# Kernel optimization log

Measured on AMD Instinct MI355X. Metric: run time of the kernel, lower is better.

## Reference

```python
import jax, jax.numpy as jnp
import numpy as np

B = 32; L = 512; D_MODEL = 512; N_LAYERS = 4
D_STATE = 64; D_CONV = 4; EXPAND = 2; HEADDIM = 64; PRED = 96
D_INNER = EXPAND * D_MODEL            # 1024
NHEADS = D_INNER // HEADDIM           # 16
CONV_DIM = D_INNER + 2 * D_STATE      # 1152
D_IN_PROJ = 2 * D_INNER + 2 * D_STATE + NHEADS  # 2192
EPS = 1e-5


def setup_inputs() -> dict:
    key = jax.random.key(0)
    ks = jax.random.split(key, 8)
    s = lambda k, shape, scale=0.02: jax.random.normal(k, shape, jnp.float32) * scale
    return {
        "x": jax.random.normal(ks[0], (B, L, D_MODEL), jnp.float32),
        "in_proj_w": s(ks[1], (N_LAYERS, D_IN_PROJ, D_MODEL)),
        "conv_w": s(ks[2], (N_LAYERS, CONV_DIM, D_CONV), 0.2),
        "conv_b": jnp.zeros((N_LAYERS, CONV_DIM), jnp.float32),
        "dt_bias": jnp.log(jnp.expm1(jax.random.uniform(ks[3], (N_LAYERS, NHEADS), minval=0.001, maxval=0.1))),
        "A_log": jnp.log(jax.random.uniform(ks[4], (N_LAYERS, NHEADS), minval=1.0, maxval=16.0)),
        "Dp": jnp.ones((N_LAYERS, NHEADS), jnp.float32),
        "norm_w": jnp.ones((N_LAYERS, D_INNER), jnp.float32),
        "out_proj_w": s(ks[5], (N_LAYERS, D_MODEL, D_INNER)),
        "ln_w": jnp.ones((N_LAYERS, D_MODEL), jnp.float32),
        "ln_b": jnp.zeros((N_LAYERS, D_MODEL), jnp.float32),
        "final_w": s(ks[6], (D_MODEL, D_MODEL)),
        "final_b": jnp.zeros((D_MODEL,), jnp.float32),
    }


def _silu(x):
    return x * jax.nn.sigmoid(x)


def _causal_dwconv(x, w, b):
    # x: (B, L, C); depthwise causal conv, kernel D_CONV, left pad D_CONV-1
    xt = jnp.swapaxes(x, 1, 2)  # (B, C, L)
    y = jax.lax.conv_general_dilated(
        xt, w[:, None, :], window_strides=(1,), padding=[(D_CONV - 1, 0)],
        feature_group_count=CONV_DIM, dimension_numbers=("NCH", "OIH", "NCH"))
    return jnp.swapaxes(y + b[None, :, None], 1, 2)


def _ssd_scan(xh, dt, Bm, Cm, A, Dp):
    # xh: (B,L,H,P), dt: (B,L,H), Bm/Cm: (B,L,N), A/Dp: (H,)
    dA = jnp.exp(dt * A)  # (B,L,H)

    def step(h, t):
        dA_t, x_t, dt_t, B_t, C_t = t  # (B,H), (B,H,P), (B,H), (B,N), (B,N)
        h = h * dA_t[:, :, None, None] + (dt_t[:, :, None] * x_t)[..., None] * B_t[:, None, None, :]
        y = jnp.einsum("bhpn,bn->bhp", h, C_t)
        return h, y

    Bb, Ll, H, P = xh.shape
    N = Bm.shape[-1]
    h0 = jnp.zeros((Bb, H, P, N), xh.dtype)
    xs = (jnp.moveaxis(dA, 1, 0), jnp.moveaxis(xh, 1, 0), jnp.moveaxis(dt, 1, 0),
          jnp.moveaxis(Bm, 1, 0), jnp.moveaxis(Cm, 1, 0))
    _, ys = jax.lax.scan(step, h0, xs)
    y = jnp.moveaxis(ys, 0, 1)  # (B,L,H,P)
    return y + xh * Dp[None, None, :, None]


def _mamba2(x, w_in, cw, cb, dtb, a_log, dp, nw, w_out):
    zxbcdt = jnp.einsum("bld,ed->ble", x, w_in)  # (B,L,D_IN_PROJ)
    z = zxbcdt[..., :D_INNER]
    xBC = zxbcdt[..., D_INNER:D_INNER + CONV_DIM]
    dt = jax.nn.softplus(zxbcdt[..., -NHEADS:] + dtb)
    xBC = _silu(_causal_dwconv(xBC, cw, cb))
    xh = xBC[..., :D_INNER].reshape(x.shape[0], x.shape[1], NHEADS, HEADDIM)
    Bm = xBC[..., D_INNER:D_INNER + D_STATE]
    Cm = xBC[..., D_INNER + D_STATE:]
    A = -jnp.exp(a_log)
    y = _ssd_scan(xh, dt, Bm, Cm, A, dp).reshape(x.shape[0], x.shape[1], D_INNER)
    # gated RMSNorm (norm_before_gate=False): gate first, then normalize
    y = y * _silu(z)
    y = y * jax.lax.rsqrt(jnp.mean(y * y, axis=-1, keepdims=True) + EPS) * nw
    return jnp.einsum("ble,de->bld", y, w_out)


def _layernorm(x, w, b):
    xc = x - jnp.mean(x, axis=-1, keepdims=True)
    return xc * jax.lax.rsqrt(jnp.mean(xc * xc, axis=-1, keepdims=True) + EPS) * w + b


def reference(x, in_proj_w, conv_w, conv_b, dt_bias, A_log, Dp, norm_w,
              out_proj_w, ln_w, ln_b, final_w, final_b):
    h = x
    for i in range(N_LAYERS):
        res = h
        h = _mamba2(h, in_proj_w[i], conv_w[i], conv_b[i], dt_bias[i],
                    A_log[i], Dp[i], norm_w[i], out_proj_w[i])
        h = _layernorm(h + res, ln_w[i], ln_b[i])
        # dropout is identity in eval mode
    h = h[:, -PRED:, :]
    return jnp.einsum("bld,ed->ble", h, final_w) + final_b
```

## Files before the change

kernel.cpp:

```cpp
#include <hip/hip_runtime.h>
#include <stdint.h>

#define BATCH 32
#define SEQ   512
#define DM    512
#define NL    4
#define DSTATE 64
#define DI    1024
#define NH    16
#define HD    64
#define PREDN 96
#define CDIM  1152
#define CSEG  144
#define DPROJ 2192
#define XBW   1168
#define NC    8
#define EPSF  1e-5f

typedef float  f32x4  __attribute__((ext_vector_type(4)));
typedef __bf16 bf16x4 __attribute__((ext_vector_type(4)));
typedef __bf16 bf16x8 __attribute__((ext_vector_type(8)));

__device__ __forceinline__ float sigmoidf_(float x){ return 1.f/(1.f+__expf(-x)); }
__device__ __forceinline__ float siluf_(float x){ return x*sigmoidf_(x); }
__device__ __forceinline__ float softplusf_(float x){ return (x>20.f)?x:log1pf(__expf(x)); }

__device__ __forceinline__ void gld16(const void* g, void* l){
  __builtin_amdgcn_global_load_lds((__attribute__((address_space(1))) void*)g,
                                   (__attribute__((address_space(3))) void*)l, 16, 0, 0);
}

template<typename TC>
__global__ __launch_bounds__(256) void gemm128(
    const __bf16* __restrict__ A, const __bf16* __restrict__ W,
    TC* __restrict__ C, TC* __restrict__ C2, const float* __restrict__ bias,
    int M, int Nreal, int ldc, int ldc2, int splitN, int K, int remapA)
{
  __shared__ __bf16 sAB[2*128*64];
  __bf16* sA = sAB;
  __bf16* sW = sAB + 128*64;
  const int tid  = threadIdx.x;
  const int m0   = blockIdx.x*128, n0 = blockIdx.y*128;
  const int lane = tid&63, wave = tid>>6;
  const int l15  = lane&15, quad = lane>>4;
  const int wr   = (wave>>1)*64, wc = (wave&1)*64;
  f32x4 acc[4][4];
  #pragma unroll
  for (int a=0;a<4;++a)
    #pragma unroll
    for (int b=0;b<4;++b) acc[a][b] = (f32x4){0,0,0,0};

  for (int k0=0; k0<K; k0+=64){
    #pragma unroll
    for (int j=0;j<4;++j){
      const int f = j*256 + tid;
      const int r = f>>3;
      const int kc = (((f&7) ^ (r&7)))*8;
      int ga = m0 + r;
      if (remapA){ int bb = ga/PREDN; ga = bb*SEQ + (SEQ-PREDN) + (ga - bb*PREDN); }
      gld16(A + (size_t)ga*K + k0 + kc, &sA[f*8]);
      int rb = n0 + r; rb = rb < Nreal ? rb : (Nreal-1);
      gld16(W + (size_t)rb*K + k0 + kc, &sW[f*8]);
    }
    __syncthreads();
    #pragma unroll
    for (int kk=0; kk<64; kk+=32){
      const int kcb = (kk>>3) + quad;
      bf16x8 av[4], bv[4];
      #pragma unroll
      for (int mi=0;mi<4;++mi){
        const int row = wr+mi*16+l15;
        av[mi] = *(const bf16x8*)&sA[row*64 + ((kcb ^ (row&7))<<3)];
      }
      #pragma unroll
      for (int ni=0;ni<4;++ni){
        const int row = wc+ni*16+l15;
        bv[ni] = *(const bf16x8*)&sW[row*64 + ((kcb ^ (row&7))<<3)];
      }
      #pragma unroll
      for (int mi=0;mi<4;++mi)
        #pragma unroll
        for (int ni=0;ni<4;++ni)
          acc[mi][ni] = __builtin_amdgcn_mfma_f32_16x16x32_bf16(av[mi],bv[ni],acc[mi][ni],0,0,0);
    }
    __syncthreads();
  }

  if constexpr (sizeof(TC)==2){
    #pragma unroll
    for (int mi=0;mi<4;++mi)
      #pragma unroll
      for (int ni=0;ni<4;++ni)
        #pragma unroll
        for (int r4=0;r4<4;++r4){
          const int row = wr+mi*16+quad*4+r4;
          const int col = wc+ni*16+l15;
          const int g2  = (col>>3) ^ (row&15);
          sAB[row*128 + g2*8 + (col&7)] = (__bf16)acc[mi][ni][r4];
        }
    __syncthreads();
    #pragma unroll
    for (int it=0; it<8; ++it){
      const int idx = it*256 + tid;
      const int row = idx>>4, g = idx&15;
      const int g2 = g ^ (row&15);
      bf16x8 v = *(const bf16x8*)&sAB[row*128 + g2*8];
      const int col0 = n0 + g*8;
      if (col0 < Nreal){
        const int grow = m0 + row;
        if (col0 < splitN) *(bf16x8*)&C [(size_t)grow*ldc  + col0]          = v;
        else               *(bf16x8*)&C2[(size_t)grow*ldc2 + (col0-splitN)] = v;
      }
    }
  } else {
    #pragma unroll
    for (int ni=0;ni<4;++ni){
      const int col = n0 + wc + ni*16 + l15;
      if (col < Nreal){
        const float badd = bias ? bias[col] : 0.f;
        #pragma unroll
        for (int mi=0;mi<4;++mi){
          #pragma unroll
          for (int r4=0;r4<4;++r4){
            const int row = m0 + wr + mi*16 + quad*4 + r4;
            C[(size_t)row*ldc + col] = (TC)(acc[mi][ni][r4] + badd);
          }
        }
      }
    }
  }
}

__global__ __launch_bounds__(256) void cast4_k(
    const float* __restrict__ s0, __bf16* __restrict__ d0, int n0,
    const float* __restrict__ s1, __bf16* __restrict__ d1, int n1,
    const float* __restrict__ s2, __bf16* __restrict__ d2, int n2,
    const float* __restrict__ s3, __bf16* __restrict__ d3, int n3)
{
  int i = blockIdx.x*256 + threadIdx.x;
  const float* s; __bf16* d;
  if (i < n0){ s=s0; d=d0; }
  else if ((i-=n0) < n1){ s=s1; d=d1; }
  else if ((i-=n1) < n2){ s=s2; d=d2; }
  else if ((i-=n2) < n3){ s=s3; d=d3; }
  else return;
  float4 v = ((const float4*)s)[i];
  bf16x4 o;
  o[0]=(__bf16)v.x; o[1]=(__bf16)v.y; o[2]=(__bf16)v.z; o[3]=(__bf16)v.w;
  ((bf16x4*)d)[i] = o;
}

__global__ __launch_bounds__(256) void conv_silu_k(
    const __bf16* __restrict__ xbw, const float* __restrict__ cw,
    const float* __restrict__ cb, __bf16* __restrict__ xout,
    __bf16* __restrict__ bcout)
{
  int idx = blockIdx.x*256 + threadIdx.x;
  if (idx >= BATCH*SEQ*CSEG) return;
  const int seg = idx % CSEG;
  const int bt  = idx / CSEG;
  const int t = bt % SEQ, b = bt / SEQ;
  const int d0 = seg*8;
  const __bf16* src = xbw + ((size_t)b*SEQ + t)*XBW + d0;
  bf16x8 z8;
  #pragma unroll
  for (int e=0;e<8;++e) z8[e]=(__bf16)0.f;
  bf16x8 x3 = *(const bf16x8*)src;
  bf16x8 x2 = (t>=1)? *(const bf16x8*)(src -   XBW) : z8;
  bf16x8 x1 = (t>=2)? *(const bf16x8*)(src - 2*XBW) : z8;
  bf16x8 x0 = (t>=3)? *(const bf16x8*)(src - 3*XBW) : z8;
  const float4* w4  = (const float4*)(cw + (size_t)d0*4);
  const float4* cb4 = (const float4*)(cb + d0);
  float4 cbl = cb4[0], cbh = cb4[1];
  bf16x8 o;
  #pragma unroll
  for (int e=0;e<8;++e){
    float4 w = w4[e];
    float acc = (e<4 ? (&cbl.x)[e] : (&cbh.x)[e-4])
              + w.x*(float)x0[e] + w.y*(float)x1[e]
              + w.z*(float)x2[e] + w.w*(float)x3[e];
    o[e] = (__bf16)siluf_(acc);
  }
  if (d0 < DI) *(bf16x8*)(xout  + ((size_t)b*SEQ+t)*DI  + d0)       = o;
  else         *(bf16x8*)(bcout + ((size_t)b*SEQ+t)*128 + (d0-DI))  = o;
}

__global__ __launch_bounds__(256) void ssd_fused_k(
    const __bf16* __restrict__ bc,
    __bf16* __restrict__ xy,
    const __bf16* __restrict__ xbw,
    const float* __restrict__ dtb_, const float* __restrict__ alog_,
    const float* __restrict__ dp_)
{
  __shared__ __bf16 sPool[5*64*72];
  __bf16* sB   = sPool;
  __bf16* sS   = sPool;
  __bf16* sC   = sPool + 1*64*72;
  __bf16* sXT  = sPool + 2*64*72;
  __bf16* sBwT = sPool + 3*64*72;
  __bf16* sHT  = sPool + 4*64*72;
  __shared__ float sCS[SEQ], sDT[SEQ];
  const int bid = blockIdx.x;
  const int h = bid & 15, b = bid >> 4;
  const int tid = threadIdx.x, wave = tid>>6, lane = tid&63;
  const int l15 = lane&15, quad = lane>>4;
  const int wm = (wave>>1)*32, wn = (wave&1)*32;

  const float Ah  = -__expf(alog_[h]);
  const float dtb = dtb_[h];
  const float Dh  = dp_[h];

  for (int t = tid; t < SEQ; t += 256){
    float raw = (float)xbw[((size_t)b*SEQ + t)*XBW + CDIM + h];
    float dt = softplusf_(raw + dtb);
    sDT[t] = dt;
    sCS[t] = dt*Ah;
  }
  __syncthreads();
  for (int ch = wave; ch < NC; ch += 4){
    float s = sCS[ch*64 + lane];
    #pragma unroll
    for (int off=1; off<64; off<<=1){
      float v = __shfl_up(s, off);
      if (lane >= off) s += v;
    }
    sCS[ch*64 + lane] = s;
  }
  __syncthreads();

  f32x4 run[2][2];
  #pragma unroll
  for (int a=0;a<2;++a)
    #pragma unroll
    for (int d=0;d<2;++d) run[a][d] = (f32x4){0,0,0,0};

  for (int c = 0; c < NC; ++c){
    const int t0 = c*64;
    {
      const int r = tid>>2, seg = (tid&3)*16;
      const __bf16* row = bc + ((size_t)b*SEQ + t0 + r)*128;
      bf16x8 vb0 = *(const bf16x8*)(row + seg);
      bf16x8 vb1 = *(const bf16x8*)(row + seg + 8);
      bf16x8 vc0 = *(const bf16x8*)(row + 64 + seg);
      bf16x8 vc1 = *(const bf16x8*)(row + 64 + seg + 8);
      *(bf16x8*)&sB[r*72+seg]   = vb0;
      *(bf16x8*)&sB[r*72+seg+8] = vb1;
      *(bf16x8*)&sC[r*72+seg]   = vc0;
      *(bf16x8*)&sC[r*72+seg+8] = vc1;
      const float w = __expf(sCS[t0+63] - sCS[t0+r]) * sDT[t0+r];
      #pragma unroll
      for (int e=0;e<8;++e){
        sBwT[(seg+e)*72 + r]   = (__bf16)(w*(float)vb0[e]);
        sBwT[(seg+8+e)*72 + r] = (__bf16)(w*(float)vb1[e]);
      }
      const __bf16* xrow = xy + ((size_t)b*SEQ + t0 + r)*DI + h*64;
      bf16x8 vx0 = *(const bf16x8*)(xrow + seg);
      bf16x8 vx1 = *(const bf16x8*)(xrow + seg + 8);
      #pragma unroll
      for (int e=0;e<8;++e){
        sXT[(seg+e)*72 + r]   = vx0[e];
        sXT[(seg+8+e)*72 + r] = vx1[e];
      }
    }
    __syncthreads();

    f32x4 aS[2][2];
    #pragma unroll
    for (int a=0;a<2;++a)
      #pragma unroll
      for (int d=0;d<2;++d) aS[a][d] = (f32x4){0,0,0,0};
    #pragma unroll
    for (int kk=0; kk<64; kk+=32){
      const int kf = kk + quad*8;
      bf16x8 a0 = *(const bf16x8*)&sC[(wm+l15)*72+kf];
      bf16x8 a1 = *(const bf16x8*)&sC[(wm+16+l15)*72+kf];
      bf16x8 b0 = *(const bf16x8*)&sB[(wn+l15)*72+kf];
      bf16x8 b1 = *(const bf16x8*)&sB[(wn+16+l15)*72+kf];
      aS[0][0] = __builtin_amdgcn_mfma_f32_16x16x32_bf16(a0,b0,aS[0][0],0,0,0);
      aS[0][1] = __builtin_amdgcn_mfma_f32_16x16x32_bf16(a0,b1,aS[0][1],0,0,0);
      aS[1][0] = __builtin_amdgcn_mfma_f32_16x16x32_bf16(a1,b0,aS[1][0],0,0,0);
      aS[1][1] = __builtin_amdgcn_mfma_f32_16x16x32_bf16(a1,b1,aS[1][1],0,0,0);
    }
    __syncthreads();

    #pragma unroll
    for (int mi=0;mi<2;++mi)
      #pragma unroll
      for (int ni=0;ni<2;++ni)
        #pragma unroll
        for (int r4=0;r4<4;++r4){
          const int i = wm+mi*16+quad*4+r4, j = wn+ni*16+l15;
          float ed = __expf(fminf(sCS[t0+i]-sCS[t0+j], 0.f)) * sDT[t0+j];
          float v = aS[mi][ni][r4]*ed;
          sS[i*72+j] = (__bf16)((j<=i)? v : 0.f);
          sHT[j*72+i] = (__bf16)run[mi][ni][r4];
        }
    __syncthreads();

    f32x4 aY[2][2], aH[2][2], aYi[2][2];
    #pragma unroll
    for (int a=0;a<2;++a)
      #pragma unroll
      for (int d=0;d<2;++d){
        aY[a][d]=(f32x4){0,0,0,0}; aH[a][d]=(f32x4){0,0,0,0};
        aYi[a][d]=(f32x4){0,0,0,0};
      }
    #pragma unroll
    for (int kk=0; kk<64; kk+=32){
      const int kf = kk + quad*8;
      bf16x8 b0 = *(const bf16x8*)&sXT[(wn+l15)*72+kf];
      bf16x8 b1 = *(const bf16x8*)&sXT[(wn+16+l15)*72+kf];
      bf16x8 s0 = *(const bf16x8*)&sS[(wm+l15)*72+kf];
      bf16x8 s1 = *(const bf16x8*)&sS[(wm+16+l15)*72+kf];
      bf16x8 w0 = *(const bf16x8*)&sBwT[(wm+l15)*72+kf];
      bf16x8 w1 = *(const bf16x8*)&sBwT[(wm+16+l15)*72+kf];
      bf16x8 c0 = *(const bf16x8*)&sC[(wm+l15)*72+kf];
      bf16x8 c1 = *(const bf16x8*)&sC[(wm+16+l15)*72+kf];
      bf16x8 h0 = *(const bf16x8*)&sHT[(wn+l15)*72+kf];
      bf16x8 h1 = *(const bf16x8*)&sHT[(wn+16+l15)*72+kf];
      aY[0][0] = __builtin_amdgcn_mfma_f32_16x16x32_bf16(s0,b0,aY[0][0],0,0,0);
      aY[0][1] = __builtin_amdgcn_mfma_f32_16x16x32_bf16(s0,b1,aY[0][1],0,0,0);
      aY[1][0] = __builtin_amdgcn_mfma_f32_16x16x32_bf16(s1,b0,aY[1][0],0,0,0);
      aY[1][1] = __builtin_amdgcn_mfma_f32_16x16x32_bf16(s1,b1,aY[1][1],0,0,0);
      aH[0][0] = __builtin_amdgcn_mfma_f32_16x16x32_bf16(w0,b0,aH[0][0],0,0,0);
      aH[0][1] = __builtin_amdgcn_mfma_f32_16x16x32_bf16(w0,b1,aH[0][1],0,0,0);
      aH[1][0] = __builtin_amdgcn_mfma_f32_16x16x32_bf16(w1,b0,aH[1][0],0,0,0);
      aH[1][1] = __builtin_amdgcn_mfma_f32_16x16x32_bf16(w1,b1,aH[1][1],0,0,0);
      aYi[0][0] = __builtin_amdgcn_mfma_f32_16x16x32_bf16(c0,h0,aYi[0][0],0,0,0);
      aYi[0][1] = __builtin_amdgcn_mfma_f32_16x16x32_bf16(c0,h1,aYi[0][1],0,0,0);
      aYi[1][0] = __builtin_amdgcn_mfma_f32_16x16x32_bf16(c1,h0,aYi[1][0],0,0,0);
      aYi[1][1] = __builtin_amdgcn_mfma_f32_16x16x32_bf16(c1,h1,aYi[1][1],0,0,0);
    }

    const float lam = __expf(sCS[t0+63]);
    #pragma unroll
    for (int mi=0;mi<2;++mi)
      #pragma unroll
      for (int ni=0;ni<2;++ni)
        #pragma unroll
        for (int r4=0;r4<4;++r4){
          const int i = wm+mi*16+quad*4+r4;
          const int p = wn+ni*16+l15;
          const float xval = (float)sXT[p*72 + i];
          const float e2 = __expf(sCS[t0+i]);
          const float yv = aY[mi][ni][r4] + Dh*xval + e2*aYi[mi][ni][r4];
          xy[((size_t)b*SEQ + t0 + i)*DI + h*64 + p] = (__bf16)yv;
          run[mi][ni][r4] = run[mi][ni][r4]*lam + aH[mi][ni][r4];
        }
    __syncthreads();
  }
}

__global__ __launch_bounds__(256) void gate_rms_k(
    __bf16* __restrict__ y, const __bf16* __restrict__ z, const float* __restrict__ nw)
{
  __shared__ float red[4];
  const int tid = threadIdx.x;
  const int sub = tid>>7;
  const int off = (tid&127)*8;
  const size_t row = (size_t)blockIdx.x*2 + sub;
  __bf16* yrow = y + row*DI;
  const __bf16* zrow = z + row*DI;
  bf16x8 yv = *(const bf16x8*)(yrow+off);
  bf16x8 zv = *(const bf16x8*)(zrow+off);
  float u[8]; float ss = 0.f;
  #pragma unroll
  for (int e=0;e<8;++e){
    float uu = (float)yv[e]*siluf_((float)zv[e]);
    u[e]=uu; ss += uu*uu;
  }
  #pragma unroll
  for (int o=32;o;o>>=1) ss += __shfl_xor(ss,o);
  if ((tid&63)==0) red[tid>>6] = ss;
  __syncthreads();
  ss = red[sub*2] + red[sub*2+1];
  const float sc = rsqrtf(ss*(1.f/DI) + EPSF);
  const float4* nw4 = (const float4*)(nw + off);
  float4 n0 = nw4[0], n1 = nw4[1];
  bf16x8 o;
  #pragma unroll
  for (int e=0;e<8;++e)
    o[e] = (__bf16)(u[e]*sc*(e<4 ? (&n0.x)[e] : (&n1.x)[e-4]));
  *(bf16x8*)(yrow+off) = o;
}

__global__ __launch_bounds__(256) void add_ln_k(
    const __bf16* __restrict__ tmp, __bf16* __restrict__ resio,
    const float* __restrict__ w, const float* __restrict__ bb)
{
  const int tid = threadIdx.x, lane = tid&63;
  const size_t row = (size_t)blockIdx.x*4 + (tid>>6);
  const int off = lane*8;
  const __bf16* trow = tmp + row*DM;
  __bf16* rrow = resio + row*DM;
  bf16x8 tv = *(const bf16x8*)(trow+off);
  bf16x8 rv = *(const bf16x8*)(rrow+off);
  float v[8]; float s = 0.f;
  #pragma unroll
  for (int e=0;e<8;++e){ v[e]=(float)tv[e]+(float)rv[e]; s += v[e]; }
  #pragma unroll
  for (int o=32;o;o>>=1) s += __shfl_xor(s,o);
  const float mean = s*(1.f/DM);
  float q = 0.f;
  #pragma unroll
  for (int e=0;e<8;++e){ v[e]-=mean; q += v[e]*v[e]; }
  #pragma unroll
  for (int o=32;o;o>>=1) q += __shfl_xor(q,o);
  const float rstd = rsqrtf(q*(1.f/DM) + EPSF);
  const float4* w4 = (const float4*)(w + off);
  const float4* b4 = (const float4*)(bb + off);
  float4 w0=w4[0], w1=w4[1], b0=b4[0], b1=b4[1];
  bf16x8 o8;
  #pragma unroll
  for (int e=0;e<8;++e){
    float we = e<4 ? (&w0.x)[e] : (&w1.x)[e-4];
    float be = e<4 ? (&b0.x)[e] : (&b1.x)[e-4];
    o8[e] = (__bf16)(v[e]*rstd*we + be);
  }
  *(bf16x8*)(rrow+off) = o8;
}

extern "C" void kernel_launch(void* const* d_in, const int* in_sizes, int n_in,
                              void* d_out, int out_size, void* d_ws, size_t ws_size,
                              hipStream_t stream)
{
  const float* x         = (const float*)d_in[0];
  const float* in_proj_w = (const float*)d_in[1];
  const float* conv_w    = (const float*)d_in[2];
  const float* conv_b    = (const float*)d_in[3];
  const float* dt_bias   = (const float*)d_in[4];
  const float* A_log     = (const float*)d_in[5];
  const float* Dp        = (const float*)d_in[6];
  const float* norm_w    = (const float*)d_in[7];
  const float* out_proj_w= (const float*)d_in[8];
  const float* ln_w      = (const float*)d_in[9];
  const float* ln_b      = (const float*)d_in[10];
  const float* final_w   = (const float*)d_in[11];
  const float* final_b   = (const float*)d_in[12];
  float* out = (float*)d_out;

  const size_t ROWS = (size_t)BATCH*SEQ;
  __bf16* wbf_in  = (__bf16*)d_ws;
  __bf16* wbf_out = wbf_in  + (size_t)NL*DPROJ*DM;
  __bf16* wbf_fin = wbf_out + (size_t)NL*DM*DI;
  __bf16* zbuf    = wbf_fin + (size_t)DM*DM;
  __bf16* xbw     = zbuf    + ROWS*DI;
  __bf16* ybuf    = xbw     + ROWS*XBW;
  __bf16* bcb     = ybuf    + ROWS*DI;
  __bf16* xcur    = bcb     + ROWS*128;
  __bf16* tmp  = xbw;

  {
    int n1 = NL*DPROJ*DM/4, n2 = NL*DM*DI/4, n3 = DM*DM/4, n4 = (int)(ROWS*DM/4);
    int tot = n1+n2+n3+n4;
    cast4_k<<<(tot+255)/256, 256, 0, stream>>>(
        in_proj_w, wbf_in, n1, out_proj_w, wbf_out, n2,
        final_w, wbf_fin, n3, x, xcur, n4);
  }

  const int convTotal = BATCH*SEQ*CSEG;
  const int BIGN = 1<<30;

  for (int l=0; l<NL; ++l){
    const __bf16* wl = wbf_in + (size_t)l*DPROJ*DM;
    gemm128<__bf16><<<dim3((int)(ROWS/128), (DPROJ+127)/128), 256, 0, stream>>>(
        xcur, wl, zbuf, xbw, nullptr, (int)ROWS, DPROJ, DI, XBW, DI, DM, 0);
    conv_silu_k<<<(convTotal+255)/256, 256, 0, stream>>>(
        xbw, conv_w + (size_t)l*CDIM*4, conv_b + (size_t)l*CDIM, ybuf, bcb);
    ssd_fused_k<<<BATCH*NH, 256, 0, stream>>>(
        bcb, ybuf, xbw, dt_bias + l*NH, A_log + l*NH, Dp + l*NH);
    gate_rms_k<<<(int)(ROWS/2), 256, 0, stream>>>(ybuf, zbuf, norm_w + (size_t)l*DI);
    gemm128<__bf16><<<dim3((int)(ROWS/128), DM/128), 256, 0, stream>>>(
        ybuf, wbf_out + (size_t)l*DM*DI, tmp, tmp, nullptr, (int)ROWS, DM, DM, DM, BIGN, DI, 0);
    add_ln_k<<<(int)(ROWS/4), 256, 0, stream>>>(tmp, xcur, ln_w + l*DM, ln_b + l*DM);
  }
  gemm128<float><<<dim3((BATCH*PREDN)/128, DM/128), 256, 0, stream>>>(
      xcur, wbf_fin, out, out, final_b, BATCH*PREDN, DM, DM, DM, BIGN, DM, 1);
}
```

Baseline: 835.5 us.

## Fuse gated RMSNorm into SSD epilogue and out-projection GEMM

```diff
diff --git a/kernel.cpp b/kernel.cpp
--- a/kernel.cpp
+++ b/kernel.cpp
@@ -34,6 +34,7 @@
 __global__ __launch_bounds__(256) void gemm128(
     const __bf16* __restrict__ A, const __bf16* __restrict__ W,
     TC* __restrict__ C, TC* __restrict__ C2, const float* __restrict__ bias,
+    const float* __restrict__ rowscale,
     int M, int Nreal, int ldc, int ldc2, int splitN, int K, int remapA)
 {
   __shared__ __bf16 sAB[2*128*64];
@@ -108,6 +109,11 @@
       const int col0 = n0 + g*8;
       if (col0 < Nreal){
         const int grow = m0 + row;
+        if (rowscale){
+          const float s = rsqrtf(rowscale[grow]*(1.f/DI) + EPSF);
+          #pragma unroll
+          for (int e=0;e<8;++e) v[e] = (__bf16)((float)v[e]*s);
+        }
         if (col0 < splitN) *(bf16x8*)&C [(size_t)grow*ldc  + col0]          = v;
         else               *(bf16x8*)&C2[(size_t)grow*ldc2 + (col0-splitN)] = v;
       }
@@ -131,23 +137,46 @@
   }
 }
 
-__global__ __launch_bounds__(256) void cast4_k(
+__global__ __launch_bounds__(256) void cast5_k(
     const float* __restrict__ s0, __bf16* __restrict__ d0, int n0,
     const float* __restrict__ s1, __bf16* __restrict__ d1, int n1,
+    const float* __restrict__ nw_,
     const float* __restrict__ s2, __bf16* __restrict__ d2, int n2,
-    const float* __restrict__ s3, __bf16* __restrict__ d3, int n3)
+    const float* __restrict__ s3, __bf16* __restrict__ d3, int n3,
+    float* __restrict__ z4, int n4)
 {
   int i = blockIdx.x*256 + threadIdx.x;
-  const float* s; __bf16* d;
-  if (i < n0){ s=s0; d=d0; }
-  else if ((i-=n0) < n1){ s=s1; d=d1; }
-  else if ((i-=n1) < n2){ s=s2; d=d2; }
-  else if ((i-=n2) < n3){ s=s3; d=d3; }
-  else return;
-  float4 v = ((const float4*)s)[i];
-  bf16x4 o;
-  o[0]=(__bf16)v.x; o[1]=(__bf16)v.y; o[2]=(__bf16)v.z; o[3]=(__bf16)v.w;
-  ((bf16x4*)d)[i] = o;
+  if (i < n0){
+    float4 v = ((const float4*)s0)[i];
+    bf16x4 o; o[0]=(__bf16)v.x; o[1]=(__bf16)v.y; o[2]=(__bf16)v.z; o[3]=(__bf16)v.w;
+    ((bf16x4*)d0)[i] = o; return;
+  }
+  i -= n0;
+  if (i < n1){
+    float4 v = ((const float4*)s1)[i];
+    const int flat = i*4;
+    const int l = flat / (DM*DI);
+    const int k = flat % DI;
+    float4 w = *(const float4*)(nw_ + l*DI + k);
+    bf16x4 o;
+    o[0]=(__bf16)(v.x*w.x); o[1]=(__bf16)(v.y*w.y);
+    o[2]=(__bf16)(v.z*w.z); o[3]=(__bf16)(v.w*w.w);
+    ((bf16x4*)d1)[i] = o; return;
+  }
+  i -= n1;
+  if (i < n2){
+    float4 v = ((const float4*)s2)[i];
+    bf16x4 o; o[0]=(__bf16)v.x; o[1]=(__bf16)v.y; o[2]=(__bf16)v.z; o[3]=(__bf16)v.w;
+    ((bf16x4*)d2)[i] = o; return;
+  }
+  i -= n2;
+  if (i < n3){
+    float4 v = ((const float4*)s3)[i];
+    bf16x4 o; o[0]=(__bf16)v.x; o[1]=(__bf16)v.y; o[2]=(__bf16)v.z; o[3]=(__bf16)v.w;
+    ((bf16x4*)d3)[i] = o; return;
+  }
+  i -= n3;
+  if (i < n4) ((float4*)z4)[i] = (float4){0,0,0,0};
 }
 
 __global__ __launch_bounds__(256) void conv_silu_k(
@@ -189,8 +218,9 @@
     const __bf16* __restrict__ bc,
     __bf16* __restrict__ xy,
     const __bf16* __restrict__ xbw,
+    const __bf16* __restrict__ zg,
     const float* __restrict__ dtb_, const float* __restrict__ alog_,
-    const float* __restrict__ dp_)
+    const float* __restrict__ dp_, float* __restrict__ gss)
 {
   __shared__ __bf16 sPool[5*64*72];
   __bf16* sB   = sPool;
@@ -200,6 +230,7 @@
   __bf16* sBwT = sPool + 3*64*72;
   __bf16* sHT  = sPool + 4*64*72;
   __shared__ float sCS[SEQ], sDT[SEQ];
+  __shared__ float sU2[64];
   const int bid = blockIdx.x;
   const int h = bid & 15, b = bid >> 4;
   const int tid = threadIdx.x, wave = tid>>6, lane = tid&63;
@@ -216,6 +247,7 @@
     sDT[t] = dt;
     sCS[t] = dt*Ah;
   }
+  if (tid < 64) sU2[tid] = 0.f;
   __syncthreads();
   for (int ch = wave; ch < NC; ch += 4){
     float s = sCS[ch*64 + lane];
@@ -333,6 +365,11 @@
     }
 
     const float lam = __expf(sCS[t0+63]);
+    float usq[2][4];
+    #pragma unroll
+    for (int mi=0;mi<2;++mi)
+      #pragma unroll
+      for (int r4=0;r4<4;++r4) usq[mi][r4] = 0.f;
     #pragma unroll
     for (int mi=0;mi<2;++mi)
       #pragma unroll
@@ -344,44 +381,28 @@
           const float xval = (float)sXT[p*72 + i];
           const float e2 = __expf(sCS[t0+i]);
           const float yv = aY[mi][ni][r4] + Dh*xval + e2*aYi[mi][ni][r4];
-          xy[((size_t)b*SEQ + t0 + i)*DI + h*64 + p] = (__bf16)yv;
+          const size_t gidx = ((size_t)b*SEQ + t0 + i)*DI + h*64 + p;
+          const float zf = (float)zg[gidx];
+          const float u = yv * siluf_(zf);
+          xy[gidx] = (__bf16)u;
+          usq[mi][r4] += u*u;
           run[mi][ni][r4] = run[mi][ni][r4]*lam + aH[mi][ni][r4];
         }
-    __syncthreads();
-  }
-}
-
-__global__ __launch_bounds__(256) void gate_rms_k(
-    __bf16* __restrict__ y, const __bf16* __restrict__ z, const float* __restrict__ nw)
-{
-  __shared__ float red[4];
-  const int tid = threadIdx.x;
-  const int sub = tid>>7;
-  const int off = (tid&127)*8;
-  const size_t row = (size_t)blockIdx.x*2 + sub;
-  __bf16* yrow = y + row*DI;
-  const __bf16* zrow = z + row*DI;
-  bf16x8 yv = *(const bf16x8*)(yrow+off);
-  bf16x8 zv = *(const bf16x8*)(zrow+off);
-  float u[8]; float ss = 0.f;
-  #pragma unroll
-  for (int e=0;e<8;++e){
-    float uu = (float)yv[e]*siluf_((float)zv[e]);
-    u[e]=uu; ss += uu*uu;
-  }
-  #pragma unroll
-  for (int o=32;o;o>>=1) ss += __shfl_xor(ss,o);
-  if ((tid&63)==0) red[tid>>6] = ss;
-  __syncthreads();
-  ss = red[sub*2] + red[sub*2+1];
-  const float sc = rsqrtf(ss*(1.f/DI) + EPSF);
-  const float4* nw4 = (const float4*)(nw + off);
-  float4 n0 = nw4[0], n1 = nw4[1];
-  bf16x8 o;
-  #pragma unroll
-  for (int e=0;e<8;++e)
-    o[e] = (__bf16)(u[e]*sc*(e<4 ? (&n0.x)[e] : (&n1.x)[e-4]));
-  *(bf16x8*)(yrow+off) = o;
+    #pragma unroll
+    for (int mi=0;mi<2;++mi)
+      #pragma unroll
+      for (int r4=0;r4<4;++r4){
+        float s = usq[mi][r4];
+        s += __shfl_xor(s, 1); s += __shfl_xor(s, 2);
+        s += __shfl_xor(s, 4); s += __shfl_xor(s, 8);
+        if (l15 == 0) atomicAdd(&sU2[wm+mi*16+quad*4+r4], s);
+      }
+    __syncthreads();
+    if (tid < 64){
+      atomicAdd(&gss[(size_t)b*SEQ + t0 + tid], sU2[tid]);
+      sU2[tid] = 0.f;
+    }
+  }
 }
 
 __global__ __launch_bounds__(256) void add_ln_k(
@@ -448,14 +469,18 @@
   __bf16* ybuf    = xbw     + ROWS*XBW;
   __bf16* bcb     = ybuf    + ROWS*DI;
   __bf16* xcur    = bcb     + ROWS*128;
+  float*  gss     = (float*)(xcur + ROWS*DM);
   __bf16* tmp  = xbw;
 
   {
     int n1 = NL*DPROJ*DM/4, n2 = NL*DM*DI/4, n3 = DM*DM/4, n4 = (int)(ROWS*DM/4);
-    int tot = n1+n2+n3+n4;
-    cast4_k<<<(tot+255)/256, 256, 0, stream>>>(
-        in_proj_w, wbf_in, n1, out_proj_w, wbf_out, n2,
-        final_w, wbf_fin, n3, x, xcur, n4);
+    int n5 = NL*(int)ROWS/4;
+    int tot = n1+n2+n3+n4+n5;
+    cast5_k<<<(tot+255)/256, 256, 0, stream>>>(
+        in_proj_w, wbf_in, n1,
+        out_proj_w, wbf_out, n2, norm_w,
+        final_w, wbf_fin, n3, x, xcur, n4,
+        gss, n5);
   }
 
   const int convTotal = BATCH*SEQ*CSEG;
@@ -463,17 +488,18 @@
 
   for (int l=0; l<NL; ++l){
     const __bf16* wl = wbf_in + (size_t)l*DPROJ*DM;
+    float* gss_l = gss + (size_t)l*ROWS;
     gemm128<__bf16><<<dim3((int)(ROWS/128), (DPROJ+127)/128), 256, 0, stream>>>(
-        xcur, wl, zbuf, xbw, nullptr, (int)ROWS, DPROJ, DI, XBW, DI, DM, 0);
+        xcur, wl, zbuf, xbw, nullptr, nullptr, (int)ROWS, DPROJ, DI, XBW, DI, DM, 0);
     conv_silu_k<<<(convTotal+255)/256, 256, 0, stream>>>(
         xbw, conv_w + (size_t)l*CDIM*4, conv_b + (size_t)l*CDIM, ybuf, bcb);
     ssd_fused_k<<<BATCH*NH, 256, 0, stream>>>(
-        bcb, ybuf, xbw, dt_bias + l*NH, A_log + l*NH, Dp + l*NH);
-    gate_rms_k<<<(int)(ROWS/2), 256, 0, stream>>>(ybuf, zbuf, norm_w + (size_t)l*DI);
+        bcb, ybuf, xbw, zbuf, dt_bias + l*NH, A_log + l*NH, Dp + l*NH, gss_l);
     gemm128<__bf16><<<dim3((int)(ROWS/128), DM/128), 256, 0, stream>>>(
-        ybuf, wbf_out + (size_t)l*DM*DI, tmp, tmp, nullptr, (int)ROWS, DM, DM, DM, BIGN, DI, 0);
+        ybuf, wbf_out + (size_t)l*DM*DI, tmp, tmp, nullptr, gss_l,
+        (int)ROWS, DM, DM, DM, BIGN, DI, 0);
     add_ln_k<<<(int)(ROWS/4), 256, 0, stream>>>(tmp, xcur, ln_w + l*DM, ln_b + l*DM);
   }
   gemm128<float><<<dim3((BATCH*PREDN)/128, DM/128), 256, 0, stream>>>(
-      xcur, wbf_fin, out, out, final_b, BATCH*PREDN, DM, DM, DM, BIGN, DM, 1);
-}
+      xcur, wbf_fin, out, out, final_b, nullptr, BATCH*PREDN, DM, DM, DM, BIGN, DM, 1);
+}
```

Result: slower. 939.3 us (+12.4%).
